# Kernel optimization log

Hardware: AMD Instinct MI355X
Metric: run time of the kernel (lower is better)

## Reference

```python
import jax, jax.numpy as jnp
import numpy as np

N_NODES = 50000


def _sage_layer(h, src, dst, W_self, W_neigh, b):
    # DGL SAGEConv with 'mean' aggregator: fc_self(h) + fc_neigh(mean_{u in N(v)} h_u) + b
    msg = h[src]                                             # [E, d] gather
    agg = jax.ops.segment_sum(msg, dst, num_segments=N_NODES)  # [N, d]
    deg = jax.ops.segment_sum(jnp.ones((src.shape[0], 1), h.dtype), dst, num_segments=N_NODES)
    mean = agg / jnp.maximum(deg, 1.0)
    return h @ W_self + mean @ W_neigh + b


def _edge_mlp(h, src, dst, Wp1, bp1, Wp2, bp2):
    # MLPPredictor: score(u,v) = W2 relu(W1 [h_u ; h_v])
    z = jnp.concatenate([h[src], h[dst]], axis=-1)           # [Ep, 2*out]
    hdn = jax.nn.relu(z @ Wp1 + bp1)
    return (hdn @ Wp2 + bp2)[:, 0]                           # [Ep]


def setup_inputs() -> dict:
    key = jax.random.key(0)
    ks = jax.random.split(key, 16)
    N, E, EP = N_NODES, 160000, 100000
    d_in, d_h, d_out = 512, 256, 64

    def glorot(k, shape):
        fan = shape[0] + shape[1]
        return jax.random.normal(k, shape, jnp.float32) * jnp.sqrt(2.0 / fan)

    return {
        "x": jax.random.normal(ks[0], (N, d_in), jnp.float32),
        "edge_src": jax.random.randint(ks[1], (E,), 0, N, jnp.int32),
        "edge_dst": jax.random.randint(ks[2], (E,), 0, N, jnp.int32),
        "pos_src": jax.random.randint(ks[3], (EP,), 0, N, jnp.int32),
        "pos_dst": jax.random.randint(ks[4], (EP,), 0, N, jnp.int32),
        "neg_src": jax.random.randint(ks[5], (EP,), 0, N, jnp.int32),
        "neg_dst": jax.random.randint(ks[6], (EP,), 0, N, jnp.int32),
        "W_self1": glorot(ks[7], (d_in, d_h)),
        "W_neigh1": glorot(ks[8], (d_in, d_h)),
        "b1": jnp.zeros((d_h,), jnp.float32),
        "W_self2": glorot(ks[9], (d_h, d_out)),
        "W_neigh2": glorot(ks[10], (d_h, d_out)),
        "b2": jnp.zeros((d_out,), jnp.float32),
        "Wp1": glorot(ks[11], (2 * d_out, d_out)),
        "bp1": jnp.zeros((d_out,), jnp.float32),
        "Wp2": glorot(ks[12], (d_out, 1)),
        "bp2": jnp.zeros((1,), jnp.float32),
    }


def reference(x, edge_src, edge_dst, pos_src, pos_dst, neg_src, neg_dst,
              W_self1, W_neigh1, b1, W_self2, W_neigh2, b2, Wp1, bp1, Wp2, bp2):
    # 2-layer SAGE (512 -> 256 -> 64), relu between layers
    h = jax.nn.relu(_sage_layer(x, edge_src, edge_dst, W_self1, W_neigh1, b1))
    h = _sage_layer(h, edge_src, edge_dst, W_self2, W_neigh2, b2)
    pos_score = _edge_mlp(h, pos_src, pos_dst, Wp1, bp1, Wp2, bp2)
    neg_score = _edge_mlp(h, neg_src, neg_dst, Wp1, bp1, Wp2, bp2)
    return (pos_score, neg_score)
```

## Files before the change

### kernel.cpp

```cpp
#include <hip/hip_runtime.h>

#define NN 50000
#define NE 160000
#define NP 100000
#define DIN 512
#define DH  256
#define DO  64
#define NBLK_SCAN 196

#define PW1_BLKS 1024
#define PW2_BLKS 128
#define PWP_BLKS 32
#define ZDEG_BLKS 196
#define PREP_BLKS (PW1_BLKS + PW2_BLKS + PWP_BLKS + ZDEG_BLKS)

typedef short bf16x8 __attribute__((ext_vector_type(8)));
typedef float f32x4  __attribute__((ext_vector_type(4)));

__device__ __forceinline__ float bf2f(unsigned short u) {
    return __uint_as_float(((unsigned int)u) << 16);
}
__device__ __forceinline__ unsigned short f2bf(float f) {
    unsigned int x = __float_as_uint(f);
    return (unsigned short)((x + 0x7fffu + ((x >> 16) & 1u)) >> 16);
}

__device__ __forceinline__ void gload_lds16(const void* g, void* l) {
    __builtin_amdgcn_global_load_lds(
        (const __attribute__((address_space(1))) void*)g,
        (__attribute__((address_space(3))) void*)l, 16, 0, 0);
}

__global__ __launch_bounds__(256) void prep_all(
    const float* __restrict__ Wself1, const float* __restrict__ Wneigh1, unsigned short* __restrict__ Bt1,
    const float* __restrict__ Wself2, const float* __restrict__ Wneigh2, unsigned short* __restrict__ Bt2,
    const float* __restrict__ Wp1, unsigned short* __restrict__ Wp1b,
    int* __restrict__ deg_i)
{
    int blk = blockIdx.x;
    if (blk < PW1_BLKS) {
        int idx = blk * 256 + threadIdx.x;
        int n = idx >> 9, k = idx & 511;
        float v = (n < DH) ? Wself1[(size_t)k * DH + n] : Wneigh1[(size_t)k * DH + (n - DH)];
        Bt1[idx] = f2bf(v);
        return;
    }
    blk -= PW1_BLKS;
    if (blk < PW2_BLKS) {
        int idx = blk * 256 + threadIdx.x;
        int n = idx >> 8, k = idx & 255;
        float v = (n < DO) ? Wself2[(size_t)k * DO + n] : Wneigh2[(size_t)k * DO + (n - DO)];
        Bt2[idx] = f2bf(v);
        return;
    }
    blk -= PW2_BLKS;
    if (blk < PWP_BLKS) {
        int idx = blk * 256 + threadIdx.x;
        int n = idx >> 7, k = idx & 127;
        Wp1b[idx] = f2bf(Wp1[(size_t)k * 64 + n]);
        return;
    }
    blk -= PWP_BLKS;
    {
        int i = blk * 256 + threadIdx.x;
        if (i < 50048) deg_i[i] = 0;
    }
}

__global__ __launch_bounds__(256) void deg_count(const int* __restrict__ dst, int* __restrict__ deg) {
    int e = blockIdx.x * 256 + threadIdx.x;
    if (e < NE) atomicAdd(&deg[dst[e]], 1);
}

__global__ __launch_bounds__(256) void scan_part(const int* __restrict__ deg, int* __restrict__ excl,
                                                 int* __restrict__ bsums) {
    __shared__ int sh[256];
    int i = blockIdx.x * 256 + threadIdx.x;
    int v = (i < NN) ? deg[i] : 0;
    sh[threadIdx.x] = v;
    __syncthreads();
    #pragma unroll
    for (int off = 1; off < 256; off <<= 1) {
        int t = (threadIdx.x >= off) ? sh[threadIdx.x - off] : 0;
        __syncthreads();
        sh[threadIdx.x] += t;
        __syncthreads();
    }
    if (i < NN) excl[i] = sh[threadIdx.x] - v;
    if (threadIdx.x == 255) bsums[blockIdx.x] = sh[255];
}

__global__ __launch_bounds__(256) void scan_sums(int* __restrict__ bsums, int* __restrict__ boff) {
    __shared__ int sh[256];
    int v = (threadIdx.x < NBLK_SCAN) ? bsums[threadIdx.x] : 0;
    sh[threadIdx.x] = v;
    __syncthreads();
    #pragma unroll
    for (int off = 1; off < 256; off <<= 1) {
        int t = (threadIdx.x >= off) ? sh[threadIdx.x - off] : 0;
        __syncthreads();
        sh[threadIdx.x] += t;
        __syncthreads();
    }
    boff[threadIdx.x] = sh[threadIdx.x] - v;
}

__global__ __launch_bounds__(256) void scan_add(int* __restrict__ off, const int* __restrict__ boff,
                                                int* __restrict__ cursor) {
    int i = blockIdx.x * 256 + threadIdx.x;
    if (i < NN) {
        int o = off[i] + boff[blockIdx.x];
        off[i] = o;
        cursor[i] = o;
    }
    if (i == 0) off[NN] = NE;
}

__global__ __launch_bounds__(256) void fill_csr(const int* __restrict__ src, const int* __restrict__ dst,
                                                int* __restrict__ cursor, int* __restrict__ eidx) {
    int e = blockIdx.x * 256 + threadIdx.x;
    if (e < NE) {
        int p = atomicAdd(&cursor[dst[e]], 1);
        eidx[p] = src[e];
    }
}

__global__ __launch_bounds__(256) void gemm_xf32(
    const float* __restrict__ A, const unsigned short* __restrict__ Bt,
    unsigned short* __restrict__ Cout, int M, int N, int K)
{
    __shared__ unsigned short As[128 * 64];
    __shared__ unsigned short Bs[128 * 64];
    const int tid = threadIdx.x;
    const int w = tid >> 6, l = tid & 63;
    const int wr = (w >> 1) * 64, wc = (w & 1) * 64;

    const int nwg = gridDim.x, gx = N >> 7;
    const int q = nwg >> 3, r = nwg & 7;
    const int xcd = blockIdx.x & 7, pos = blockIdx.x >> 3;
    const int work = (xcd < r ? xcd * (q + 1) : r * (q + 1) + (xcd - r) * q) + pos;
    const int row0 = (work / gx) * 128, col0 = (work % gx) * 128;

    f32x4 acc[4][4];
    #pragma unroll
    for (int i = 0; i < 4; ++i)
        #pragma unroll
        for (int j = 0; j < 4; ++j)
            #pragma unroll
            for (int rr = 0; rr < 4; ++rr) acc[i][j][rr] = 0.0f;

    const int wave_lds_chunk = (tid & 192) * 8;

    float4 pa[4][2];
    #pragma unroll
    for (int u = 0; u < 4; ++u) {
        int c = u * 256 + tid;
        int row = c >> 3, j = c & 7;
        int grow = row0 + row; if (grow >= M) grow = M - 1;
        const float* s = A + (size_t)grow * K + j * 8;
        pa[u][0] = *(const float4*)s;
        pa[u][1] = *(const float4*)(s + 4);
    }

    for (int k0 = 0; k0 < K; k0 += 64) {
        __syncthreads();
        #pragma unroll
        for (int u = 0; u < 4; ++u) {
            int c = u * 256 + tid;
            int cn = c >> 3, j = c & 7;
            int js = j ^ (cn & 7);
            gload_lds16(Bt + (size_t)(col0 + cn) * K + k0 + js * 8,
                        (void*)(Bs + (u * 256) * 8 + wave_lds_chunk));
        }
        #pragma unroll
        for (int u = 0; u < 4; ++u) {
            int c = u * 256 + tid;
            int row = c >> 3, j = c & 7;
            int js = j ^ (row & 7);
            union { bf16x8 v; unsigned int u32[4]; } pk;
            asm("v_cvt_pk_bf16_f32 %0, %1, %2" : "=v"(pk.u32[0]) : "v"(pa[u][0].x), "v"(pa[u][0].y));
            asm("v_cvt_pk_bf16_f32 %0, %1, %2" : "=v"(pk.u32[1]) : "v"(pa[u][0].z), "v"(pa[u][0].w));
            asm("v_cvt_pk_bf16_f32 %0, %1, %2" : "=v"(pk.u32[2]) : "v"(pa[u][1].x), "v"(pa[u][1].y));
            asm("v_cvt_pk_bf16_f32 %0, %1, %2" : "=v"(pk.u32[3]) : "v"(pa[u][1].z), "v"(pa[u][1].w));
            *(bf16x8*)&As[row * 64 + js * 8] = pk.v;
        }
        __syncthreads();

        if (k0 + 64 < K) {
            #pragma unroll
            for (int u = 0; u < 4; ++u) {
                int c = u * 256 + tid;
                int row = c >> 3, j = c & 7;
                int grow = row0 + row; if (grow >= M) grow = M - 1;
                const float* s = A + (size_t)grow * K + (k0 + 64) + j * 8;
                pa[u][0] = *(const float4*)s;
                pa[u][1] = *(const float4*)(s + 4);
            }
        }

        #pragma unroll
        for (int kk = 0; kk < 2; ++kk) {
            bf16x8 af[4], bfv[4];
            #pragma unroll
            for (int i = 0; i < 4; ++i) {
                int row = wr + i * 16 + (l & 15);
                int ch = (kk * 4 + (l >> 4)) ^ (row & 7);
                af[i] = *(const bf16x8*)&As[row * 64 + ch * 8];
            }
            #pragma unroll
            for (int j = 0; j < 4; ++j) {
                int cc = wc + j * 16 + (l & 15);
                int ch = (kk * 4 + (l >> 4)) ^ (cc & 7);
                bfv[j] = *(const bf16x8*)&Bs[cc * 64 + ch * 8];
            }
            #pragma unroll
            for (int i = 0; i < 4; ++i)
                #pragma unroll
                for (int j = 0; j < 4; ++j)
                    acc[i][j] = __builtin_amdgcn_mfma_f32_16x16x32_bf16(af[i], bfv[j], acc[i][j], 0, 0, 0);
        }
    }

    #pragma unroll
    for (int i = 0; i < 4; ++i) {
        #pragma unroll
        for (int j = 0; j < 4; ++j) {
            int r0 = row0 + wr + i * 16 + ((l >> 4) << 2);
            int c  = col0 + wc + j * 16 + (l & 15);
            #pragma unroll
            for (int rr = 0; rr < 4; ++rr) {
                if (r0 + rr < M)
                    Cout[(size_t)(r0 + rr) * N + c] = f2bf(acc[i][j][rr]);
            }
        }
    }
}

__global__ __launch_bounds__(256) void gemm_bf16(
    const unsigned short* __restrict__ A, const unsigned short* __restrict__ Bt,
    unsigned short* __restrict__ Cout, int M, int N, int K)
{
    __shared__ unsigned short As[128 * 64];
    __shared__ unsigned short Bs[128 * 64];
    const int tid = threadIdx.x;
    const int w = tid >> 6, l = tid & 63;
    const int wr = (w >> 1) * 64, wc = (w & 1) * 64;

    const int nwg = gridDim.x, gx = N >> 7;
    const int q = nwg >> 3, r = nwg & 7;
    const int xcd = blockIdx.x & 7, pos = blockIdx.x >> 3;
    const int work = (xcd < r ? xcd * (q + 1) : r * (q + 1) + (xcd - r) * q) + pos;
    const int row0 = (work / gx) * 128, col0 = (work % gx) * 128;

    f32x4 acc[4][4];
    #pragma unroll
    for (int i = 0; i < 4; ++i)
        #pragma unroll
        for (int j = 0; j < 4; ++j)
            #pragma unroll
            for (int rr = 0; rr < 4; ++rr) acc[i][j][rr] = 0.0f;

    const int wave_lds_chunk = (tid & 192) * 8;

    for (int k0 = 0; k0 < K; k0 += 64) {
        __syncthreads();
        #pragma unroll
        for (int u = 0; u < 4; ++u) {
            int c = u * 256 + tid;
            int row = c >> 3, j = c & 7;
            int js = j ^ (row & 7);
            int grow = row0 + row; if (grow >= M) grow = M - 1;
            gload_lds16(A + (size_t)grow * K + k0 + js * 8,
                        (void*)(As + (u * 256) * 8 + wave_lds_chunk));
        }
        #pragma unroll
        for (int u = 0; u < 4; ++u) {
            int c = u * 256 + tid;
            int cn = c >> 3, j = c & 7;
            int js = j ^ (cn & 7);
            gload_lds16(Bt + (size_t)(col0 + cn) * K + k0 + js * 8,
                        (void*)(Bs + (u * 256) * 8 + wave_lds_chunk));
        }
        __syncthreads();

        #pragma unroll
        for (int kk = 0; kk < 2; ++kk) {
            bf16x8 af[4], bfv[4];
            #pragma unroll
            for (int i = 0; i < 4; ++i) {
                int row = wr + i * 16 + (l & 15);
                int ch = (kk * 4 + (l >> 4)) ^ (row & 7);
                af[i] = *(const bf16x8*)&As[row * 64 + ch * 8];
            }
            #pragma unroll
            for (int j = 0; j < 4; ++j) {
                int cc = wc + j * 16 + (l & 15);
                int ch = (kk * 4 + (l >> 4)) ^ (cc & 7);
                bfv[j] = *(const bf16x8*)&Bs[cc * 64 + ch * 8];
            }
            #pragma unroll
            for (int i = 0; i < 4; ++i)
                #pragma unroll
                for (int j = 0; j < 4; ++j)
                    acc[i][j] = __builtin_amdgcn_mfma_f32_16x16x32_bf16(af[i], bfv[j], acc[i][j], 0, 0, 0);
        }
    }

    #pragma unroll
    for (int i = 0; i < 4; ++i) {
        #pragma unroll
        for (int j = 0; j < 4; ++j) {
            int r0 = row0 + wr + i * 16 + ((l >> 4) << 2);
            int c  = col0 + wc + j * 16 + (l & 15);
            #pragma unroll
            for (int rr = 0; rr < 4; ++rr) {
                if (r0 + rr < M)
                    Cout[(size_t)(r0 + rr) * N + c] = f2bf(acc[i][j][rr]);
            }
        }
    }
}

__global__ __launch_bounds__(256) void agg_combine256(
    const unsigned short* __restrict__ C1, const int* __restrict__ off, const int* __restrict__ eidx,
    const float* __restrict__ b, unsigned short* __restrict__ h1b)
{
    const int wave = threadIdx.x >> 6, lane = threadIdx.x & 63;
    const int n = blockIdx.x * 4 + wave;
    if (n >= NN) return;
    const int e0 = off[n], e1 = off[n + 1];
    float acc0 = 0.f, acc1 = 0.f, acc2 = 0.f, acc3 = 0.f;
    for (int e = e0; e < e1; ++e) {
        int s = eidx[e];
        ushort4 v = *(const ushort4*)&C1[(size_t)s * 512 + 256 + lane * 4];
        acc0 += bf2f(v.x); acc1 += bf2f(v.y); acc2 += bf2f(v.z); acc3 += bf2f(v.w);
    }
    const float rd = (e1 > e0) ? 1.0f / (float)(e1 - e0) : 1.0f;
    ushort4 sv = *(const ushort4*)&C1[(size_t)n * 512 + lane * 4];
    float4 bb = ((const float4*)b)[lane];
    ushort4 o;
    o.x = f2bf(fmaxf(bf2f(sv.x) + acc0 * rd + bb.x, 0.f));
    o.y = f2bf(fmaxf(bf2f(sv.y) + acc1 * rd + bb.y, 0.f));
    o.z = f2bf(fmaxf(bf2f(sv.z) + acc2 * rd + bb.z, 0.f));
    o.w = f2bf(fmaxf(bf2f(sv.w) + acc3 * rd + bb.w, 0.f));
    *(ushort4*)&h1b[(size_t)n * 256 + lane * 4] = o;
}

__global__ __launch_bounds__(256) void agg_combine64(
    const unsigned short* __restrict__ C2, const int* __restrict__ off, const int* __restrict__ eidx,
    const float* __restrict__ b, unsigned short* __restrict__ h2b)
{
    const int wave = threadIdx.x >> 6, lane = threadIdx.x & 63;
    const int n = blockIdx.x * 4 + wave;
    if (n >= NN) return;
    const int e0 = off[n], e1 = off[n + 1];
    float acc = 0.f;
    for (int e = e0; e < e1; ++e) {
        int s = eidx[e];
        acc += bf2f(C2[(size_t)s * 128 + 64 + lane]);
    }
    const float rd = (e1 > e0) ? 1.0f / (float)(e1 - e0) : 1.0f;
    h2b[(size_t)n * 64 + lane] = f2bf(bf2f(C2[(size_t)n * 128 + lane]) + acc * rd + b[lane]);
}

__global__ __launch_bounds__(256) void edge_mlp_mfma(
    const unsigned short* __restrict__ h2b,
    const int* __restrict__ psrc, const int* __restrict__ pdst,
    const int* __restrict__ nsrc, const int* __restrict__ ndst,
    const unsigned short* __restrict__ Wp1b, const float* __restrict__ bp1,
    const float* __restrict__ Wp2, const float* __restrict__ bp2,
    float* __restrict__ out)
{
    __shared__ unsigned short z[128 * 128];
    const int tid = threadIdx.x;
    const int w = tid >> 6, l = tid & 63;
    const int e0 = blockIdx.x * 128;

    bf16x8 bfr[4][4];
    #pragma unroll
    for (int kk = 0; kk < 4; ++kk)
        #pragma unroll
        for (int j = 0; j < 4; ++j) {
            int col = j * 16 + (l & 15);
            int ch  = kk * 4 + (l >> 4);
            bfr[kk][j] = *(const bf16x8*)(Wp1b + col * 128 + ch * 8);
        }

    #pragma unroll
    for (int p = 0; p < 8; ++p) {
        int rho = p * 32 + (tid >> 3);
        int c   = tid & 7;
        int r   = rho >> 1;
        int ep  = rho & 1;
        int e   = e0 + r; if (e >= 2 * NP) e = 2 * NP - 1;
        int node = (e < NP) ? (ep ? pdst[e] : psrc[e])
                            : (ep ? ndst[e - NP] : nsrc[e - NP]);
        bf16x8 v = *(const bf16x8*)(h2b + (size_t)node * 64 + c * 8);
        int j = ep * 8 + c;
        *(bf16x8*)&z[r * 128 + ((j ^ (r & 15)) * 8)] = v;
    }
    __syncthreads();

    f32x4 acc[2][4];
    #pragma unroll
    for (int i = 0; i < 2; ++i)
        #pragma unroll
        for (int j = 0; j < 4; ++j)
            #pragma unroll
            for (int rr = 0; rr < 4; ++rr) acc[i][j][rr] = 0.0f;

    #pragma unroll
    for (int kk = 0; kk < 4; ++kk) {
        bf16x8 af[2];
        #pragma unroll
        for (int i = 0; i < 2; ++i) {
            int row = w * 32 + i * 16 + (l & 15);
            int ch  = (kk * 4 + (l >> 4)) ^ (row & 15);
            af[i] = *(const bf16x8*)&z[row * 128 + ch * 8];
        }
        #pragma unroll
        for (int i = 0; i < 2; ++i)
            #pragma unroll
            for (int j = 0; j < 4; ++j)
                acc[i][j] = __builtin_amdgcn_mfma_f32_16x16x32_bf16(af[i], bfr[kk][j], acc[i][j], 0, 0, 0);
    }

    float bp1v[4], w2v[4];
    #pragma unroll
    for (int j = 0; j < 4; ++j) {
        bp1v[j] = bp1[j * 16 + (l & 15)];
        w2v[j]  = Wp2[j * 16 + (l & 15)];
    }
    const float b2v = bp2[0];
    #pragma unroll
    for (int i = 0; i < 2; ++i) {
        #pragma unroll
        for (int rr = 0; rr < 4; ++rr) {
            float p = 0.f;
            #pragma unroll
            for (int j = 0; j < 4; ++j) {
                float h = fmaxf(acc[i][j][rr] + bp1v[j], 0.f);
                p = fmaf(h, w2v[j], p);
            }
            #pragma unroll
            for (int off = 8; off > 0; off >>= 1)
                p += __shfl_xor(p, off, 64);
            int row = w * 32 + i * 16 + ((l >> 4) << 2) + rr;
            if ((l & 15) == 0 && e0 + row < 2 * NP)
                out[e0 + row] = p + b2v;
        }
    }
}

extern "C" void kernel_launch(void* const* d_in, const int* in_sizes, int n_in,
                              void* d_out, int out_size, void* d_ws, size_t ws_size,
                              hipStream_t stream) {
    (void)in_sizes; (void)n_in; (void)out_size; (void)ws_size;
    const float* x       = (const float*)d_in[0];
    const int*   esrc    = (const int*)d_in[1];
    const int*   edst    = (const int*)d_in[2];
    const int*   psrc    = (const int*)d_in[3];
    const int*   pdst    = (const int*)d_in[4];
    const int*   nsrc    = (const int*)d_in[5];
    const int*   ndst    = (const int*)d_in[6];
    const float* Wself1  = (const float*)d_in[7];
    const float* Wneigh1 = (const float*)d_in[8];
    const float* b1      = (const float*)d_in[9];
    const float* Wself2  = (const float*)d_in[10];
    const float* Wneigh2 = (const float*)d_in[11];
    const float* b2      = (const float*)d_in[12];
    const float* Wp1     = (const float*)d_in[13];
    const float* bp1     = (const float*)d_in[14];
    const float* Wp2     = (const float*)d_in[15];
    const float* bp2     = (const float*)d_in[16];
    float* out = (float*)d_out;

    char* w = (char*)d_ws;
    int* deg_i  = (int*)w; w += 50048 * 4;
    int* off    = (int*)w; w += 50052 * 4;
    int* cursor = (int*)w; w += 50048 * 4;
    int* bsums  = (int*)w; w += 256 * 4;
    int* boff   = (int*)w; w += 256 * 4;
    int* eidx   = (int*)w; w += 160000 * 4;
    unsigned short* Bt1  = (unsigned short*)w; w += (size_t)512 * 512 * 2;
    unsigned short* Bt2  = (unsigned short*)w; w += (size_t)128 * 256 * 2;
    unsigned short* Wp1b = (unsigned short*)w; w += (size_t)64 * 128 * 2;
    unsigned short* h1b  = (unsigned short*)w; w += (size_t)NN * DH * 2;
    unsigned short* h2b  = (unsigned short*)w; w += (size_t)NN * DO * 2;
    unsigned short* C1b  = (unsigned short*)w; w += (size_t)NN * 512 * 2;
    unsigned short* C2b  = C1b;

    prep_all<<<PREP_BLKS, 256, 0, stream>>>(Wself1, Wneigh1, Bt1,
                                            Wself2, Wneigh2, Bt2, Wp1, Wp1b, deg_i);

    deg_count<<<(NE + 255) / 256, 256, 0, stream>>>(edst, deg_i);
    scan_part<<<NBLK_SCAN, 256, 0, stream>>>(deg_i, off, bsums);
    scan_sums<<<1, 256, 0, stream>>>(bsums, boff);
    scan_add<<<NBLK_SCAN, 256, 0, stream>>>(off, boff, cursor);
    fill_csr<<<(NE + 255) / 256, 256, 0, stream>>>(esrc, edst, cursor, eidx);

    int nwg1 = (512 / 128) * ((NN + 127) / 128);
    gemm_xf32<<<nwg1, 256, 0, stream>>>(x, Bt1, C1b, NN, 512, DIN);
    agg_combine256<<<(NN + 3) / 4, 256, 0, stream>>>(C1b, off, eidx, b1, h1b);

    int nwg2 = (128 / 128) * ((NN + 127) / 128);
    gemm_bf16<<<nwg2, 256, 0, stream>>>(h1b, Bt2, C2b, NN, 128, DH);
    agg_combine64<<<(NN + 3) / 4, 256, 0, stream>>>(C2b, off, eidx, b2, h2b);

    edge_mlp_mfma<<<(2 * NP + 127) / 128, 256, 0, stream>>>(h2b, psrc, pdst, nsrc, ndst,
                                                            Wp1b, bp1, Wp2, bp2, out);
}
```

Before: 176.6 us.

## Double-buffer LDS tiles in fp32-input GEMM to overlap staging with MFMA

Turns the A and B shared-memory tiles of the fp32-input GEMM into two buffers each. The next k-step is staged (async B global-to-LDS load plus A bf16 conversion and store) while MFMAs run on the current buffer. This leaves one barrier per iteration instead of two and hides load latency behind compute. It doubles LDS use to 64KB per block, which may lower occupancy. It also adds a prefetch two tiles ahead, which holds more registers live.

```diff
diff --git a/kernel.cpp b/kernel.cpp
--- a/kernel.cpp
+++ b/kernel.cpp
@@ -129,8 +129,8 @@
     const float* __restrict__ A, const unsigned short* __restrict__ Bt,
     unsigned short* __restrict__ Cout, int M, int N, int K)
 {
-    __shared__ unsigned short As[128 * 64];
-    __shared__ unsigned short Bs[128 * 64];
+    __shared__ unsigned short As[2][128 * 64];
+    __shared__ unsigned short Bs[2][128 * 64];
     const int tid = threadIdx.x;
     const int w = tid >> 6, l = tid & 63;
     const int wr = (w >> 1) * 64, wc = (w & 1) * 64;
@@ -152,50 +152,61 @@
     const int wave_lds_chunk = (tid & 192) * 8;
 
     float4 pa[4][2];
-    #pragma unroll
-    for (int u = 0; u < 4; ++u) {
-        int c = u * 256 + tid;
-        int row = c >> 3, j = c & 7;
-        int grow = row0 + row; if (grow >= M) grow = M - 1;
-        const float* s = A + (size_t)grow * K + j * 8;
-        pa[u][0] = *(const float4*)s;
-        pa[u][1] = *(const float4*)(s + 4);
-    }
-
+
+#define LOAD_PA(K0)                                                          \
+    {                                                                        \
+        _Pragma("unroll")                                                    \
+        for (int u = 0; u < 4; ++u) {                                        \
+            int c = u * 256 + tid;                                           \
+            int row_ = c >> 3, j_ = c & 7;                                   \
+            int grow = row0 + row_; if (grow >= M) grow = M - 1;             \
+            const float* s = A + (size_t)grow * K + (K0) + j_ * 8;           \
+            pa[u][0] = *(const float4*)s;                                    \
+            pa[u][1] = *(const float4*)(s + 4);                              \
+        }                                                                    \
+    }
+
+#define WRITE_A(BUF)                                                         \
+    {                                                                        \
+        _Pragma("unroll")                                                    \
+        for (int u = 0; u < 4; ++u) {                                        \
+            int c = u * 256 + tid;                                           \
+            int row_ = c >> 3, j_ = c & 7;                                   \
+            int js_ = j_ ^ (row_ & 7);                                       \
+            union { bf16x8 v; unsigned int u32[4]; } pk;                     \
+            asm("v_cvt_pk_bf16_f32 %0, %1, %2" : "=v"(pk.u32[0]) : "v"(pa[u][0].x), "v"(pa[u][0].y)); \
+            asm("v_cvt_pk_bf16_f32 %0, %1, %2" : "=v"(pk.u32[1]) : "v"(pa[u][0].z), "v"(pa[u][0].w)); \
+            asm("v_cvt_pk_bf16_f32 %0, %1, %2" : "=v"(pk.u32[2]) : "v"(pa[u][1].x), "v"(pa[u][1].y)); \
+            asm("v_cvt_pk_bf16_f32 %0, %1, %2" : "=v"(pk.u32[3]) : "v"(pa[u][1].z), "v"(pa[u][1].w)); \
+            *(bf16x8*)&As[BUF][row_ * 64 + js_ * 8] = pk.v;                  \
+        }                                                                    \
+    }
+
+#define STAGE_B(BUF, K0)                                                     \
+    {                                                                        \
+        _Pragma("unroll")                                                    \
+        for (int u = 0; u < 4; ++u) {                                        \
+            int c = u * 256 + tid;                                           \
+            int cn = c >> 3, j_ = c & 7;                                     \
+            int js_ = j_ ^ (cn & 7);                                         \
+            gload_lds16(Bt + (size_t)(col0 + cn) * K + (K0) + js_ * 8,       \
+                        (void*)(Bs[BUF] + (u * 256) * 8 + wave_lds_chunk));  \
+        }                                                                    \
+    }
+
+    LOAD_PA(0);
+    STAGE_B(0, 0);
+    WRITE_A(0);
+    LOAD_PA(64);
+    __syncthreads();
+
+    int cur = 0;
     for (int k0 = 0; k0 < K; k0 += 64) {
-        __syncthreads();
-        #pragma unroll
-        for (int u = 0; u < 4; ++u) {
-            int c = u * 256 + tid;
-            int cn = c >> 3, j = c & 7;
-            int js = j ^ (cn & 7);
-            gload_lds16(Bt + (size_t)(col0 + cn) * K + k0 + js * 8,
-                        (void*)(Bs + (u * 256) * 8 + wave_lds_chunk));
-        }
-        #pragma unroll
-        for (int u = 0; u < 4; ++u) {
-            int c = u * 256 + tid;
-            int row = c >> 3, j = c & 7;
-            int js = j ^ (row & 7);
-            union { bf16x8 v; unsigned int u32[4]; } pk;
-            asm("v_cvt_pk_bf16_f32 %0, %1, %2" : "=v"(pk.u32[0]) : "v"(pa[u][0].x), "v"(pa[u][0].y));
-            asm("v_cvt_pk_bf16_f32 %0, %1, %2" : "=v"(pk.u32[1]) : "v"(pa[u][0].z), "v"(pa[u][0].w));
-            asm("v_cvt_pk_bf16_f32 %0, %1, %2" : "=v"(pk.u32[2]) : "v"(pa[u][1].x), "v"(pa[u][1].y));
-            asm("v_cvt_pk_bf16_f32 %0, %1, %2" : "=v"(pk.u32[3]) : "v"(pa[u][1].z), "v"(pa[u][1].w));
-            *(bf16x8*)&As[row * 64 + js * 8] = pk.v;
-        }
-        __syncthreads();
-
-        if (k0 + 64 < K) {
-            #pragma unroll
-            for (int u = 0; u < 4; ++u) {
-                int c = u * 256 + tid;
-                int row = c >> 3, j = c & 7;
-                int grow = row0 + row; if (grow >= M) grow = M - 1;
-                const float* s = A + (size_t)grow * K + (k0 + 64) + j * 8;
-                pa[u][0] = *(const float4*)s;
-                pa[u][1] = *(const float4*)(s + 4);
-            }
+        const int nxt = k0 + 64;
+        if (nxt < K) {
+            STAGE_B(cur ^ 1, nxt);
+            WRITE_A(cur ^ 1);
+            if (nxt + 64 < K) LOAD_PA(nxt + 64);
         }
 
         #pragma unroll
@@ -205,13 +216,13 @@
             for (int i = 0; i < 4; ++i) {
                 int row = wr + i * 16 + (l & 15);
                 int ch = (kk * 4 + (l >> 4)) ^ (row & 7);
-                af[i] = *(const bf16x8*)&As[row * 64 + ch * 8];
+                af[i] = *(const bf16x8*)&As[cur][row * 64 + ch * 8];
             }
             #pragma unroll
             for (int j = 0; j < 4; ++j) {
                 int cc = wc + j * 16 + (l & 15);
                 int ch = (kk * 4 + (l >> 4)) ^ (cc & 7);
-                bfv[j] = *(const bf16x8*)&Bs[cc * 64 + ch * 8];
+                bfv[j] = *(const bf16x8*)&Bs[cur][cc * 64 + ch * 8];
             }
             #pragma unroll
             for (int i = 0; i < 4; ++i)
@@ -219,7 +230,12 @@
                 for (int j = 0; j < 4; ++j)
                     acc[i][j] = __builtin_amdgcn_mfma_f32_16x16x32_bf16(af[i], bfv[j], acc[i][j], 0, 0, 0);
         }
-    }
+        __syncthreads();
+        cur ^= 1;
+    }
+#undef LOAD_PA
+#undef WRITE_A
+#undef STAGE_B
 
     #pragma unroll
     for (int i = 0; i < 4; ++i) {
```

New measurement: 184.0 us. 1.04x slower.
